# Kernel tuning notes

Hardware: AMD Instinct MI355X
Metric: run time of the kernel (lower is better)

## Reference

```python
import jax, jax.numpy as jnp
import numpy as np

B, H, W, DIM, WS, SHIFT, NH = 8, 64, 64, 512, 8, 4, 16
NC, NE, HID, GH = 3, 4, 2048, 256
N = WS * WS
nW = (H // WS) * (W // WS)
HD = DIM // NH
LN_EPS = 1e-5


def _static_buffers():
    # SwinV2 log-spaced continuous relative coords table
    r = np.arange(-(WS - 1), WS, dtype=np.float32)
    table = np.stack(np.meshgrid(r, r, indexing='ij'), axis=-1)[None]  # (1,2WS-1,2WS-1,2)
    table = table / (WS - 1) * 8.0
    table = np.sign(table) * np.log2(np.abs(table) + 1.0) / np.log2(8.0)
    # relative position index (N,N)
    coords = np.stack(np.meshgrid(np.arange(WS), np.arange(WS), indexing='ij'))
    cf = coords.reshape(2, -1)
    rel = (cf[:, :, None] - cf[:, None, :]).transpose(1, 2, 0).astype(np.int64)
    rel[..., 0] += WS - 1
    rel[..., 1] += WS - 1
    rel[..., 0] *= 2 * WS - 1
    rpi = rel.sum(-1)
    # shifted-window attention mask (nW,N,N)
    img = np.zeros((1, H, W, 1), np.float32)
    cnt = 0
    sls = (slice(0, -WS), slice(-WS, -SHIFT), slice(-SHIFT, None))
    for hs in sls:
        for ws_ in sls:
            img[:, hs, ws_, :] = cnt
            cnt += 1
    mw = img.reshape(1, H // WS, WS, W // WS, WS, 1).transpose(0, 1, 3, 2, 4, 5).reshape(-1, N)
    am = mw[:, None, :] - mw[:, :, None]
    am = np.where(am != 0, -100.0, 0.0).astype(np.float32)
    return jnp.asarray(table), rpi, jnp.asarray(am)

TABLE, RPI, ATTN_MASK = _static_buffers()


def _ln(x, w, b):
    m = x.mean(-1, keepdims=True)
    v = ((x - m) ** 2).mean(-1, keepdims=True)
    return (x - m) / jnp.sqrt(v + LN_EPS) * w + b


def setup_inputs():
    key = jax.random.key(0)
    ks = iter(jax.random.split(key, 40))
    p = lambda shape: jax.random.normal(next(ks), shape, jnp.float32) * 0.02
    return {
        'x': jax.random.normal(next(ks), (B, H * W, DIM), jnp.float32),
        'qkv_w': p((3 * DIM, DIM)), 'q_bias': p((DIM,)), 'v_bias': p((DIM,)),
        'logit_scale': jnp.log(10.0 * jnp.ones((NH, 1, 1), jnp.float32)),
        'cpb_w1': p((512, 2)), 'cpb_b1': p((512,)), 'cpb_w2': p((NH, 512)),
        'proj_w': p((DIM, DIM)), 'proj_b': jnp.zeros((DIM,), jnp.float32),
        'norm1_w': jnp.ones((DIM,), jnp.float32), 'norm1_b': jnp.zeros((DIM,), jnp.float32),
        'norm2_w': jnp.ones((DIM,), jnp.float32), 'norm2_b': jnp.zeros((DIM,), jnp.float32),
        'exp_w1': p((NE, HID, DIM)), 'exp_b1': jnp.zeros((NE, HID), jnp.float32),
        'exp_w2': p((NE, DIM, HID)), 'exp_b2': jnp.zeros((NE, DIM), jnp.float32),
        'gate_l1_w': p((GH, DIM)), 'gate_l1_b': jnp.zeros((GH,), jnp.float32),
        'gate_fa_w': p((GH, GH)), 'gate_fa_b': jnp.zeros((GH,), jnp.float32),
        'gate_l2_w': p((NE, GH)), 'gate_l2_b': jnp.zeros((NE,), jnp.float32),
        'task_w': p((DIM, DIM)), 'task_b': jnp.zeros((DIM,), jnp.float32),
    }


def reference(x, qkv_w, q_bias, v_bias, logit_scale, cpb_w1, cpb_b1, cpb_w2,
              proj_w, proj_b, norm1_w, norm1_b, norm2_w, norm2_b,
              exp_w1, exp_b1, exp_w2, exp_b2,
              gate_l1_w, gate_l1_b, gate_fa_w, gate_fa_b, gate_l2_w, gate_l2_b,
              task_w, task_b):
    shortcut = x
    # cyclic shift + window partition
    xi = jnp.roll(x.reshape(B, H, W, DIM), (-SHIFT, -SHIFT), axis=(1, 2))
    xw = xi.reshape(B, H // WS, WS, W // WS, WS, DIM).transpose(0, 1, 3, 2, 4, 5).reshape(-1, N, DIM)
    # qkv with q/v bias only (k bias zero)
    qkv_b = jnp.concatenate([q_bias, jnp.zeros_like(v_bias), v_bias])
    qkv = (xw @ qkv_w.T + qkv_b).reshape(-1, N, 3, NH, HD).transpose(2, 0, 3, 1, 4)
    q, k, v = qkv[0], qkv[1], qkv[2]
    # SwinV2 cosine attention
    qn = q / jnp.maximum(jnp.linalg.norm(q, axis=-1, keepdims=True), 1e-12)
    kn = k / jnp.maximum(jnp.linalg.norm(k, axis=-1, keepdims=True), 1e-12)
    scale = jnp.exp(jnp.minimum(logit_scale, jnp.log(100.0)))
    attn = jnp.einsum('bhnd,bhmd->bhnm', qn, kn) * scale
    # continuous relative position bias
    bias_tbl = (jax.nn.relu(TABLE @ cpb_w1.T + cpb_b1) @ cpb_w2.T).reshape(-1, NH)
    rpb = bias_tbl[RPI.reshape(-1)].reshape(N, N, NH).transpose(2, 0, 1)
    attn = attn + (16.0 * jax.nn.sigmoid(rpb))[None]
    # shifted window mask
    attn = attn.reshape(B, nW, NH, N, N) + ATTN_MASK[None, :, None]
    attn = jax.nn.softmax(attn.reshape(-1, NH, N, N), axis=-1)
    out = jnp.einsum('bhnm,bhmd->bnhd', attn, v).reshape(-1, N, DIM)
    out = out @ proj_w.T + proj_b
    # window reverse + reverse shift
    xr = out.reshape(B, H // WS, W // WS, WS, WS, DIM).transpose(0, 1, 3, 2, 4, 5).reshape(B, H, W, DIM)
    xr = jnp.roll(xr, (SHIFT, SHIFT), axis=(1, 2)).reshape(B, H * W, DIM)
    x1 = shortcut + _ln(xr, norm1_w, norm1_b)  # SwinV2 post-norm residual
    # MMoE FFN (inference gating path; dropouts are eval no-ops)
    eo = []
    for e in range(NE):
        h = jax.nn.gelu(x1 @ exp_w1[e].T + exp_b1[e], approximate=False)
        eo.append(h @ exp_w2[e].T + exp_b2[e])
    eo = jnp.stack(eo, axis=-1)  # (B, L, DIM, NE)
    t = x1 @ task_w.T + task_b
    g = jax.nn.relu(t @ gate_l1_w.T + gate_l1_b)
    aw = jax.nn.softmax(g @ gate_fa_w.T + gate_fa_b, axis=-1)
    gate_logits = (g * aw) @ gate_l2_w.T + gate_l2_b
    wts = jax.nn.softmax(gate_logits, axis=-1)  # temperature = 1.0
    moe = jnp.einsum('blde,ble->bld', eo, wts)
    return x1 + _ln(moe, norm2_w, norm2_b)
```

## Files before the change

kernel.cpp:

```cpp
#include <hip/hip_runtime.h>
#include <math.h>

typedef __bf16 bf16;
typedef bf16 bf16x8 __attribute__((ext_vector_type(8)));
typedef bf16 bf16x4_t __attribute__((ext_vector_type(4)));
typedef float f32x4 __attribute__((ext_vector_type(4)));


#define EPI_QKV  0
#define EPI_PROJ 1
#define EPI_BF16 2
#define EPI_RELU 3
#define EPI_F32  4
#define EPI_GELU 5
#define EPI_MOE  6

#define NIN 26

#define GLDS16(gp, lp)                                                    \
    __builtin_amdgcn_global_load_lds(                                     \
        (const __attribute__((address_space(1))) void*)(gp),              \
        (__attribute__((address_space(3))) void*)(lp), 16, 0, 0)

__global__ __launch_bounds__(256) void probe_k(const unsigned short* __restrict__ x,
                                               int* __restrict__ flag)
{
    __shared__ int cnt[256];
    int t = threadIdx.x;
    int bad = 0;
    for (int j = t; j < 4096; j += 256) {
        int e = (x[j] >> 7) & 0xFF;
        if (e >= 132) bad++;
    }
    cnt[t] = bad;
    __syncthreads();
    for (int s = 128; s > 0; s >>= 1) {
        if (t < s) cnt[t] += cnt[t + s];
        __syncthreads();
    }
    if (t == 0) *flag = (cnt[0] > 64) ? 1 : 0;
}

struct ConvArgs {
    const void* src[NIN];
    bf16* dst[NIN];
    int n[NIN];
};

__global__ __launch_bounds__(256) void conv_k(ConvArgs a, const int* __restrict__ flag)
{
    int i = blockIdx.y;
    int n4 = a.n[i] >> 2;
    bf16x4_t* dst = (bf16x4_t*)a.dst[i];
    int stride = gridDim.x * 256;
    if (*flag) {
        const float4* s = (const float4*)a.src[i];
        for (int j = blockIdx.x * 256 + threadIdx.x; j < n4; j += stride) {
            float4 v = s[j];
            dst[j] = (bf16x4_t){(bf16)v.x, (bf16)v.y, (bf16)v.z, (bf16)v.w};
        }
    } else {
        const bf16x4_t* s = (const bf16x4_t*)a.src[i];
        for (int j = blockIdx.x * 256 + threadIdx.x; j < n4; j += stride)
            dst[j] = s[j];
    }
}

__device__ __forceinline__ int win_remap(int r) {
    int win = r >> 6, tok = r & 63;
    int b = win >> 6, wi = win & 63;
    int h = (((wi >> 3) << 3) + (tok >> 3) + 4) & 63;
    int w = (((wi & 7) << 3) + (tok & 7) + 4) & 63;
    return (b << 12) | (h << 6) | w;
}

template<int REMAP_A, int EPI>
__global__ __launch_bounds__(256, 4) void gemm_k(
    const bf16* __restrict__ A, const bf16* __restrict__ Bw,
    void* __restrict__ Cout,
    const bf16* __restrict__ bias, const bf16* __restrict__ bias2,
    const float* __restrict__ wts, int N, int K, int eIdx, int nbm)
{
    __shared__ __attribute__((aligned(16))) bf16 As[128 * 64];
    __shared__ __attribute__((aligned(16))) bf16 Bs[128 * 64];
    const int tid = threadIdx.x;

    const int lin = blockIdx.x;
    const int nbn = N >> 7;
    const int xcd = lin & 7, s = lin >> 3;
    const int nbmx = nbm >> 3;
    const int G = nbmx < 16 ? nbmx : 16;
    const int gsz = G * nbn;
    const int gi = s / gsz, rem = s - gi * gsz;
    const int bn = rem / G, bmi = rem - bn * G;
    const int bm = xcd + 8 * (gi * G + bmi);

    const int wave = tid >> 6, lane = tid & 63;
    const int wm = (wave >> 1) << 6, wn = (wave & 1) << 6;
    const int lrow = lane & 15, quad = lane >> 4;

    const int sr = tid >> 3, sc = tid & 7;
    const int scg = sc ^ (sr & 7);
    int ga[4];
#pragma unroll
    for (int i = 0; i < 4; i++) {
        int r = bm * 128 + sr + i * 32;
        ga[i] = REMAP_A ? win_remap(r) : r;
    }
    const int brow = bn * 128 + sr;
    bf16* lA = As + tid * 8;
    bf16* lB = Bs + tid * 8;

    f32x4 acc[4][4];
#pragma unroll
    for (int i = 0; i < 4; i++)
#pragma unroll
        for (int j = 0; j < 4; j++) acc[i][j] = (f32x4){0.f, 0.f, 0.f, 0.f};

    for (int k0 = 0; k0 < K; k0 += 64) {
        __syncthreads();
#pragma unroll
        for (int i = 0; i < 4; i++) {
            GLDS16(A + (size_t)ga[i] * K + k0 + scg * 8, lA + i * 2048);
            GLDS16(Bw + (size_t)(brow + i * 32) * K + k0 + scg * 8, lB + i * 2048);
        }
        __syncthreads();
#pragma unroll
        for (int ks = 0; ks < 2; ks++) {
            bf16x8 af[4], bfr[4];
#pragma unroll
            for (int t = 0; t < 4; t++) {
                int ra = wm + t * 16 + lrow;
                af[t] = *(const bf16x8*)(&As[ra * 64 + (((ks << 2) + quad) ^ (ra & 7)) * 8]);
                int rb = wn + t * 16 + lrow;
                bfr[t] = *(const bf16x8*)(&Bs[rb * 64 + (((ks << 2) + quad) ^ (rb & 7)) * 8]);
            }
#pragma unroll
            for (int tm = 0; tm < 4; tm++)
#pragma unroll
                for (int tn = 0; tn < 4; tn++)
                    acc[tm][tn] = __builtin_amdgcn_mfma_f32_16x16x32_bf16(
                        af[tm], bfr[tn], acc[tm][tn], 0, 0, 0);
        }
    }

    const int cr0 = quad << 2, cc0 = lane & 15;
#pragma unroll
    for (int tm = 0; tm < 4; tm++) {
#pragma unroll
        for (int tn = 0; tn < 4; tn++) {
#pragma unroll
            for (int r = 0; r < 4; r++) {
                int row = bm * 128 + wm + tm * 16 + cr0 + r;
                int col = bn * 128 + wn + tn * 16 + cc0;
                float v = acc[tm][tn][r];
                if constexpr (EPI == EPI_QKV) {
                    float bv = 0.f;
                    if (col < 512) bv = (float)bias[col];
                    else if (col >= 1024) bv = (float)bias2[col - 1024];
                    ((bf16*)Cout)[(size_t)row * N + col] = (bf16)(v + bv);
                } else if constexpr (EPI == EPI_PROJ) {
                    v += (float)bias[col];
                    ((bf16*)Cout)[(size_t)win_remap(row) * N + col] = (bf16)v;
                } else if constexpr (EPI == EPI_BF16) {
                    v += (float)bias[col];
                    ((bf16*)Cout)[(size_t)row * N + col] = (bf16)v;
                } else if constexpr (EPI == EPI_RELU) {
                    v += (float)bias[col];
                    ((bf16*)Cout)[(size_t)row * N + col] = (bf16)fmaxf(v, 0.f);
                } else if constexpr (EPI == EPI_F32) {
                    v += (float)bias[col];
                    ((float*)Cout)[(size_t)row * N + col] = v;
                } else if constexpr (EPI == EPI_GELU) {
                    v += (float)bias[col];
                    float u = 1.5957691216f * v * fmaf(0.044715f * v, v, 1.0f);
                    float g = v * __builtin_amdgcn_rcpf(1.0f + __expf(-u));
                    g *= wts[(size_t)row * 4 + eIdx];
                    ((bf16*)Cout)[(size_t)row * N + col] = (bf16)g;
                } else if constexpr (EPI == EPI_MOE) {
                    float* p = &((float*)Cout)[(size_t)row * N + col];
                    if (eIdx == 0) *p = v; else *p += v;
                }
            }
        }
    }
}

__global__ __launch_bounds__(64) void cpb_k(const bf16* __restrict__ w1,
                                            const bf16* __restrict__ b1,
                                            const bf16* __restrict__ w2,
                                            float* __restrict__ tbl)
{
    int e = blockIdx.x;
    int d0 = e / 15, d1 = e % 15;
    auto f = [](int d) -> float {
        float v = (float)(d - 7) * (8.0f / 7.0f);
        float t = log2f(fabsf(v) + 1.0f) * (1.0f / 3.0f);
        return v < 0.f ? -t : (v > 0.f ? t : 0.0f);
    };
    float t0 = f(d0), t1 = f(d1);
    __shared__ float hsh[512];
    int tid = threadIdx.x;
    for (int j = tid; j < 512; j += 64) {
        float h = t0 * (float)w1[j * 2 + 0] + t1 * (float)w1[j * 2 + 1] + (float)b1[j];
        hsh[j] = fmaxf(h, 0.0f);
    }
    __syncthreads();
    if (tid < 16) {
        float sum = 0.f;
        for (int j = 0; j < 512; j++) sum += hsh[j] * (float)w2[tid * 512 + j];
        tbl[e * 16 + tid] = 16.0f / (1.0f + expf(-sum));
    }
}

#define PT 72
#define VT 72
__global__ __launch_bounds__(256) void attn_k(const bf16* __restrict__ qkv,
                                              const bf16* __restrict__ lsc,
                                              const float* __restrict__ tbl,
                                              bf16* __restrict__ aout)
{
    __shared__ __attribute__((aligned(16))) bf16 VtAll[4][32 * VT];
    __shared__ __attribute__((aligned(16))) bf16 PsAll[4][64 * PT];
    const int tid  = threadIdx.x;
    const int wave = tid >> 6, lane = tid & 63;
    const int pair = blockIdx.x * 4 + wave;
    const int win  = pair >> 4, head = pair & 15;
    bf16* Vt = VtAll[wave];
    bf16* Ps = PsAll[wave];

    const int lcol = lane & 15;
    const int quad = lane >> 4;
    const int lk   = quad << 3;

    const bf16* qbase = qkv + (size_t)(win * 64) * 1536 + head * 32;

    {
        const bf16* vp = qbase + (size_t)lane * 1536 + 1024;
        bf16x8 v0 = *(const bf16x8*)(vp);
        bf16x8 v1 = *(const bf16x8*)(vp + 8);
        bf16x8 v2 = *(const bf16x8*)(vp + 16);
        bf16x8 v3 = *(const bf16x8*)(vp + 24);
#pragma unroll
        for (int j = 0; j < 8; j++) {
            Vt[(j)      * VT + lane] = v0[j];
            Vt[(j + 8)  * VT + lane] = v1[j];
            Vt[(j + 16) * VT + lane] = v2[j];
            Vt[(j + 24) * VT + lane] = v3[j];
        }
    }

    bf16x8 qf[4], kf[4];
#pragma unroll
    for (int t = 0; t < 4; t++) {
        const bf16* qp = qbase + (size_t)(t * 16 + lcol) * 1536 + lk;
        bf16x8 q = *(const bf16x8*)qp;
        float ss = 0.f;
#pragma unroll
        for (int j = 0; j < 8; j++) { float f = (float)q[j]; ss += f * f; }
        ss += __shfl_xor(ss, 16); ss += __shfl_xor(ss, 32);
        float inv = 1.f / fmaxf(sqrtf(ss), 1e-12f);
#pragma unroll
        for (int j = 0; j < 8; j++) q[j] = (bf16)((float)q[j] * inv);
        qf[t] = q;

        const bf16* kp = qbase + (size_t)(t * 16 + lcol) * 1536 + 512 + lk;
        bf16x8 k = *(const bf16x8*)kp;
        ss = 0.f;
#pragma unroll
        for (int j = 0; j < 8; j++) { float f = (float)k[j]; ss += f * f; }
        ss += __shfl_xor(ss, 16); ss += __shfl_xor(ss, 32);
        inv = 1.f / fmaxf(sqrtf(ss), 1e-12f);
#pragma unroll
        for (int j = 0; j < 8; j++) k[j] = (bf16)((float)k[j] * inv);
        kf[t] = k;
    }

    f32x4 s[4][4];
#pragma unroll
    for (int tm = 0; tm < 4; tm++)
#pragma unroll
        for (int tn = 0; tn < 4; tn++) s[tm][tn] = (f32x4){0.f, 0.f, 0.f, 0.f};
#pragma unroll
    for (int tm = 0; tm < 4; tm++)
#pragma unroll
        for (int tn = 0; tn < 4; tn++)
            s[tm][tn] = __builtin_amdgcn_mfma_f32_16x16x32_bf16(
                qf[tm], kf[tn], s[tm][tn], 0, 0, 0);

    float scale = expf(fminf((float)lsc[head], 4.6051701860f));
    int wi = win & 63, wh = wi >> 3, ww = wi & 7;
    float rinv[4][4];
#pragma unroll
    for (int tm = 0; tm < 4; tm++) {
#pragma unroll
        for (int r = 0; r < 4; r++) {
            int m = tm * 16 + quad * 4 + r;
            int qi = m >> 3, qj = m & 7;
            int qh = wh * 8 + qi, qw = ww * 8 + qj;
            int qid = (qh < 56 ? 0 : (qh < 60 ? 1 : 2)) * 3 +
                      (qw < 56 ? 0 : (qw < 60 ? 1 : 2));
            float v[4]; float mx = -1e30f;
#pragma unroll
            for (int tn = 0; tn < 4; tn++) {
                int n = tn * 16 + lcol;
                int ki = n >> 3, kj = n & 7;
                int kh = wh * 8 + ki, kw = ww * 8 + kj;
                int kid = (kh < 56 ? 0 : (kh < 60 ? 1 : 2)) * 3 +
                          (kw < 56 ? 0 : (kw < 60 ? 1 : 2));
                float val = s[tm][tn][r] * scale
                          + tbl[((qi - ki + 7) * 15 + (qj - kj + 7)) * 16 + head];
                if (kid != qid) val -= 100.f;
                v[tn] = val;
                mx = fmaxf(mx, val);
            }
            mx = fmaxf(mx, __shfl_xor(mx, 1));
            mx = fmaxf(mx, __shfl_xor(mx, 2));
            mx = fmaxf(mx, __shfl_xor(mx, 4));
            mx = fmaxf(mx, __shfl_xor(mx, 8));
            float sum = 0.f;
#pragma unroll
            for (int tn = 0; tn < 4; tn++) {
                float p = expf(v[tn] - mx);
                v[tn] = p; sum += p;
            }
            sum += __shfl_xor(sum, 1);
            sum += __shfl_xor(sum, 2);
            sum += __shfl_xor(sum, 4);
            sum += __shfl_xor(sum, 8);
            rinv[tm][r] = 1.f / sum;
#pragma unroll
            for (int tn = 0; tn < 4; tn++)
                Ps[m * PT + tn * 16 + lcol] = (bf16)v[tn];
        }
    }
    __syncthreads();

    f32x4 o[4][2];
#pragma unroll
    for (int tm = 0; tm < 4; tm++)
#pragma unroll
        for (int tn = 0; tn < 2; tn++) o[tm][tn] = (f32x4){0.f, 0.f, 0.f, 0.f};
#pragma unroll
    for (int ks = 0; ks < 2; ks++) {
        bf16x8 af[4], vf[2];
#pragma unroll
        for (int tm = 0; tm < 4; tm++)
            af[tm] = *(const bf16x8*)(&Ps[(tm * 16 + lcol) * PT + lk + ks * 32]);
#pragma unroll
        for (int tn = 0; tn < 2; tn++)
            vf[tn] = *(const bf16x8*)(&Vt[(tn * 16 + lcol) * VT + lk + ks * 32]);
#pragma unroll
        for (int tm = 0; tm < 4; tm++)
#pragma unroll
            for (int tn = 0; tn < 2; tn++)
                o[tm][tn] = __builtin_amdgcn_mfma_f32_16x16x32_bf16(
                    af[tm], vf[tn], o[tm][tn], 0, 0, 0);
    }

    bf16* ob = aout + (size_t)(win * 64) * 512 + head * 32;
#pragma unroll
    for (int tm = 0; tm < 4; tm++)
#pragma unroll
        for (int tn = 0; tn < 2; tn++)
#pragma unroll
            for (int r = 0; r < 4; r++) {
                int m = tm * 16 + quad * 4 + r;
                ob[(size_t)m * 512 + tn * 16 + lcol] =
                    (bf16)(o[tm][tn][r] * rinv[tm][r]);
            }
}

__global__ __launch_bounds__(64) void ln_res_k(const bf16* __restrict__ xin,
                                               const bf16* __restrict__ pin,
                                               const bf16* __restrict__ w,
                                               const bf16* __restrict__ b,
                                               bf16* __restrict__ x1)
{
    int row = blockIdx.x, lane = threadIdx.x;
    bf16x8 pv = *(const bf16x8*)(pin + (size_t)row * 512 + lane * 8);
    float v[8]; float s = 0.f;
#pragma unroll
    for (int i = 0; i < 8; i++) { v[i] = (float)pv[i]; s += v[i]; }
#pragma unroll
    for (int o = 32; o >= 1; o >>= 1) s += __shfl_xor(s, o);
    float mean = s * (1.f / 512.f);
    float vv = 0.f;
#pragma unroll
    for (int i = 0; i < 8; i++) { float d = v[i] - mean; vv += d * d; }
#pragma unroll
    for (int o = 32; o >= 1; o >>= 1) vv += __shfl_xor(vv, o);
    float rstd = rsqrtf(vv * (1.f / 512.f) + 1e-5f);
    bf16x8 xv = *(const bf16x8*)(xin + (size_t)row * 512 + lane * 8);
    bf16x8 wv = *(const bf16x8*)(w + lane * 8);
    bf16x8 bv = *(const bf16x8*)(b + lane * 8);
    bf16x8 ov;
#pragma unroll
    for (int i = 0; i < 8; i++) {
        float ln = (v[i] - mean) * rstd * (float)wv[i] + (float)bv[i];
        ov[i] = (bf16)((float)xv[i] + ln);
    }
    *(bf16x8*)(x1 + (size_t)row * 512 + lane * 8) = ov;
}

__global__ __launch_bounds__(64) void final_k(const float* __restrict__ moe,
                                              const bf16* __restrict__ x1,
                                              const bf16* __restrict__ w,
                                              const bf16* __restrict__ b,
                                              const float* __restrict__ wts,
                                              const bf16* __restrict__ b2,
                                              float* __restrict__ out)
{
    int row = blockIdx.x, lane = threadIdx.x;
    float w0 = wts[row * 4 + 0], w1 = wts[row * 4 + 1],
          w2 = wts[row * 4 + 2], w3 = wts[row * 4 + 3];
    const float4* mr = (const float4*)(moe + (size_t)row * 512 + lane * 8);
    float4 m0 = mr[0], m1 = mr[1];
    float v[8] = {m0.x, m0.y, m0.z, m0.w, m1.x, m1.y, m1.z, m1.w};
    bf16x8 b20 = *(const bf16x8*)(b2 + lane * 8);
    bf16x8 b21 = *(const bf16x8*)(b2 + 512 + lane * 8);
    bf16x8 b22 = *(const bf16x8*)(b2 + 1024 + lane * 8);
    bf16x8 b23 = *(const bf16x8*)(b2 + 1536 + lane * 8);
    float s = 0.f;
#pragma unroll
    for (int i = 0; i < 8; i++) {
        v[i] += w0 * (float)b20[i] + w1 * (float)b21[i]
              + w2 * (float)b22[i] + w3 * (float)b23[i];
        s += v[i];
    }
#pragma unroll
    for (int o = 32; o >= 1; o >>= 1) s += __shfl_xor(s, o);
    float mean = s * (1.f / 512.f);
    float vv = 0.f;
#pragma unroll
    for (int i = 0; i < 8; i++) { float d = v[i] - mean; vv += d * d; }
#pragma unroll
    for (int o = 32; o >= 1; o >>= 1) vv += __shfl_xor(vv, o);
    float rstd = rsqrtf(vv * (1.f / 512.f) + 1e-5f);
    bf16x8 xv = *(const bf16x8*)(x1 + (size_t)row * 512 + lane * 8);
    bf16x8 wv = *(const bf16x8*)(w + lane * 8);
    bf16x8 bv = *(const bf16x8*)(b + lane * 8);
    float ot[8];
#pragma unroll
    for (int i = 0; i < 8; i++) {
        float ln = (v[i] - mean) * rstd * (float)wv[i] + (float)bv[i];
        ot[i] = (float)xv[i] + ln;
    }
    float4* op = (float4*)(out + (size_t)row * 512 + lane * 8);
    op[0] = (float4){ot[0], ot[1], ot[2], ot[3]};
    op[1] = (float4){ot[4], ot[5], ot[6], ot[7]};
}

__global__ __launch_bounds__(64) void gate_k(const float* __restrict__ fa,
                                             const bf16* __restrict__ g,
                                             const bf16* __restrict__ w2,
                                             const bf16* __restrict__ b2,
                                             float* __restrict__ wts)
{
    int row = blockIdx.x, lane = threadIdx.x;
    const float* fr = fa + (size_t)row * 256;
    float a[4]; float mx = -1e30f;
#pragma unroll
    for (int i = 0; i < 4; i++) { a[i] = fr[lane * 4 + i]; mx = fmaxf(mx, a[i]); }
#pragma unroll
    for (int o = 32; o >= 1; o >>= 1) mx = fmaxf(mx, __shfl_xor(mx, o));
    float sum = 0.f;
#pragma unroll
    for (int i = 0; i < 4; i++) { a[i] = expf(a[i] - mx); sum += a[i]; }
#pragma unroll
    for (int o = 32; o >= 1; o >>= 1) sum += __shfl_xor(sum, o);
    float inv = 1.f / sum;
    float gb[4];
#pragma unroll
    for (int i = 0; i < 4; i++)
        gb[i] = a[i] * inv * (float)g[(size_t)row * 256 + lane * 4 + i];
    float lg[4];
#pragma unroll
    for (int j = 0; j < 4; j++) {
        float p = 0.f;
#pragma unroll
        for (int i = 0; i < 4; i++) p += gb[i] * (float)w2[j * 256 + lane * 4 + i];
        lg[j] = p;
    }
#pragma unroll
    for (int o = 32; o >= 1; o >>= 1) {
#pragma unroll
        for (int j = 0; j < 4; j++) lg[j] += __shfl_xor(lg[j], o);
    }
    if (lane == 0) {
        float m2 = -1e30f;
#pragma unroll
        for (int j = 0; j < 4; j++) { lg[j] += (float)b2[j]; m2 = fmaxf(m2, lg[j]); }
        float s2 = 0.f; float e2[4];
#pragma unroll
        for (int j = 0; j < 4; j++) { e2[j] = expf(lg[j] - m2); s2 += e2[j]; }
#pragma unroll
        for (int j = 0; j < 4; j++) wts[(size_t)row * 4 + j] = e2[j] / s2;
    }
}

extern "C" void kernel_launch(void* const* d_in, const int* in_sizes, int n_in,
                              void* d_out, int out_size, void* d_ws, size_t ws_size,
                              hipStream_t stream)
{
    float* out = (float*)d_out;
    char* ws = (char*)d_ws;
    const size_t MB = 1024ull * 1024ull;

    static const int sizes[NIN] = {
        16777216, 786432, 512, 512, 16, 1024, 512, 8192, 262144, 512,
        512, 512, 512, 512, 4194304, 8192, 4194304, 2048,
        131072, 256, 65536, 256, 1024, 4, 262144, 512
    };
    ConvArgs ca;
    size_t off = 0;
    bf16* cp[NIN];
    for (int i = 1; i < NIN; i++) {
        cp[i] = (bf16*)(ws + off);
        off += ((size_t)sizes[i] * 2 + 255) & ~255ull;
    }
    cp[0] = (bf16*)(ws + 20 * MB);
    for (int i = 0; i < NIN; i++) {
        ca.src[i] = d_in[i];
        ca.dst[i] = cp[i];
        ca.n[i]   = sizes[i];
    }
    const bf16 *xc = cp[0], *qkv_w = cp[1], *q_bias = cp[2], *v_bias = cp[3],
               *lsc = cp[4], *cpb_w1 = cp[5], *cpb_b1 = cp[6], *cpb_w2 = cp[7],
               *proj_w = cp[8], *proj_b = cp[9], *n1w = cp[10], *n1b = cp[11],
               *n2w = cp[12], *n2b = cp[13], *exp_w1 = cp[14], *exp_b1 = cp[15],
               *exp_w2 = cp[16], *exp_b2 = cp[17], *gl1w = cp[18], *gl1b = cp[19],
               *gfaw = cp[20], *gfab = cp[21], *gl2w = cp[22], *gl2b = cp[23],
               *taskw = cp[24], *taskb = cp[25];

    bf16*  qkv   = (bf16*)(ws + 53 * MB);
    bf16*  aout  = (bf16*)(ws + 149 * MB);
    bf16*  projo = (bf16*)(ws + 53 * MB);
    bf16*  x1    = (bf16*)(ws + 20 * MB);
    bf16*  tbuf  = (bf16*)(ws + 53 * MB);
    bf16*  gbuf  = (bf16*)(ws + 85 * MB);
    float* fabuf = (float*)(ws + 101 * MB);
    int*   flag  = (int*)(ws + 181 * MB);
    float* wts   = (float*)(ws + 181 * MB + 4096);
    float* tbl   = (float*)(ws + 181 * MB + 4096 + 524288);

    const bool bigws = ws_size >= 246 * MB;
    bf16*  hid = (bf16*)(ws + 53 * MB);
    float* moe = bigws ? (float*)(ws + 182 * MB) : (float*)(ws + 117 * MB);

    probe_k<<<1, 256, 0, stream>>>((const unsigned short*)d_in[0], flag);
    conv_k<<<dim3(1024, NIN), 256, 0, stream>>>(ca, flag);

    cpb_k<<<225, 64, 0, stream>>>(cpb_w1, cpb_b1, cpb_w2, tbl);
    gemm_k<1, EPI_QKV><<<256 * 12, 256, 0, stream>>>(
        xc, qkv_w, qkv, q_bias, v_bias, nullptr, 1536, 512, 0, 256);
    attn_k<<<2048, 256, 0, stream>>>(qkv, lsc, tbl, aout);
    gemm_k<0, EPI_PROJ><<<256 * 4, 256, 0, stream>>>(
        aout, proj_w, projo, proj_b, nullptr, nullptr, 512, 512, 0, 256);
    ln_res_k<<<32768, 64, 0, stream>>>(xc, projo, n1w, n1b, x1);
    gemm_k<0, EPI_BF16><<<256 * 4, 256, 0, stream>>>(
        x1, taskw, tbuf, taskb, nullptr, nullptr, 512, 512, 0, 256);
    gemm_k<0, EPI_RELU><<<256 * 2, 256, 0, stream>>>(
        tbuf, gl1w, gbuf, gl1b, nullptr, nullptr, 256, 512, 0, 256);
    gemm_k<0, EPI_F32><<<256 * 2, 256, 0, stream>>>(
        gbuf, gfaw, fabuf, gfab, nullptr, nullptr, 256, 256, 0, 256);
    gate_k<<<32768, 64, 0, stream>>>(fabuf, gbuf, gl2w, gl2b, wts);

    if (bigws) {
        for (int e = 0; e < 4; e++) {
            gemm_k<0, EPI_GELU><<<256 * 16, 256, 0, stream>>>(
                x1, exp_w1 + (size_t)e * 2048 * 512, hid,
                exp_b1 + e * 2048, nullptr, wts, 2048, 512, e, 256);
            gemm_k<0, EPI_MOE><<<256 * 4, 256, 0, stream>>>(
                hid, exp_w2 + (size_t)e * 512 * 2048, moe,
                nullptr, nullptr, nullptr, 512, 2048, e, 256);
        }
    } else {
        for (int e = 0; e < 4; e++) {
            for (int h = 0; h < 2; h++) {
                const size_t ro = (size_t)h * 16384;
                gemm_k<0, EPI_GELU><<<128 * 16, 256, 0, stream>>>(
                    x1 + ro * 512, exp_w1 + (size_t)e * 2048 * 512, hid,
                    exp_b1 + e * 2048, nullptr, wts + ro * 4, 2048, 512, e, 128);
                gemm_k<0, EPI_MOE><<<128 * 4, 256, 0, stream>>>(
                    hid, exp_w2 + (size_t)e * 512 * 2048, moe + ro * 512,
                    nullptr, nullptr, nullptr, 512, 2048, e, 128);
            }
        }
    }
    final_k<<<32768, 64, 0, stream>>>(moe, x1, n2w, n2b, wts, exp_b2, out);
}
```

Measured before the change: 1.136 ms.

## Precompute attention bias+mask table and drop max-subtraction in window softmax

A new small kernel expands the relative-position bias and shifted-window mask into a per-(window class, head) 64x64 float table. The attention kernel reads that table with one fused multiply-add per logit, instead of recomputing region IDs and gathering from the bias table. The softmax now skips the row-max reduction and uses fast exp and reciprocal intrinsics. Attention launches become single-wave blocks, one per (window, head). Dropping the max subtraction relies on cosine logits times the clamped scale staying small enough not to overflow exp. That holds for the default scale, but the clamp allows scales up to 100, where exp can overflow.

```diff
diff --git a/kernel.cpp b/kernel.cpp
--- a/kernel.cpp
+++ b/kernel.cpp
@@ -213,21 +213,33 @@
     }
 }
 
+__global__ __launch_bounds__(256) void expand_k(const float* __restrict__ tbl,
+                                                float* __restrict__ mbt)
+{
+    int head = blockIdx.x & 15, cls = blockIdx.x >> 4;
+    int eh = cls >> 1, ew = cls & 1;
+    for (int idx = threadIdx.x; idx < 4096; idx += 256) {
+        int m = idx >> 6, n = idx & 63;
+        int qi = m >> 3, qj = m & 7, ki = n >> 3, kj = n & 7;
+        float bias = tbl[((qi - ki + 7) * 15 + (qj - kj + 7)) * 16 + head];
+        int qid = (eh ? (qi < 4 ? 1 : 2) : 0) * 3 + (ew ? (qj < 4 ? 1 : 2) : 0);
+        int kid = (eh ? (ki < 4 ? 1 : 2) : 0) * 3 + (ew ? (kj < 4 ? 1 : 2) : 0);
+        mbt[(size_t)blockIdx.x * 4096 + idx] = bias + (qid != kid ? -100.f : 0.f);
+    }
+}
+
 #define PT 72
 #define VT 72
-__global__ __launch_bounds__(256) void attn_k(const bf16* __restrict__ qkv,
-                                              const bf16* __restrict__ lsc,
-                                              const float* __restrict__ tbl,
-                                              bf16* __restrict__ aout)
-{
-    __shared__ __attribute__((aligned(16))) bf16 VtAll[4][32 * VT];
-    __shared__ __attribute__((aligned(16))) bf16 PsAll[4][64 * PT];
-    const int tid  = threadIdx.x;
-    const int wave = tid >> 6, lane = tid & 63;
-    const int pair = blockIdx.x * 4 + wave;
+__global__ __launch_bounds__(64) void attn_k(const bf16* __restrict__ qkv,
+                                             const bf16* __restrict__ lsc,
+                                             const float* __restrict__ mbt,
+                                             bf16* __restrict__ aout)
+{
+    __shared__ __attribute__((aligned(16))) bf16 Vt[32 * VT];
+    __shared__ __attribute__((aligned(16))) bf16 Ps[64 * PT];
+    const int lane = threadIdx.x;
+    const int pair = blockIdx.x;
     const int win  = pair >> 4, head = pair & 15;
-    bf16* Vt = VtAll[wave];
-    bf16* Ps = PsAll[wave];
 
     const int lcol = lane & 15;
     const int quad = lane >> 4;
@@ -290,48 +302,29 @@
 
     float scale = expf(fminf((float)lsc[head], 4.6051701860f));
     int wi = win & 63, wh = wi >> 3, ww = wi & 7;
+    const float* Tb = mbt +
+        (((size_t)(((wh == 7) ? 2 : 0) + ((ww == 7) ? 1 : 0)) * 16 + head) << 12);
     float rinv[4][4];
 #pragma unroll
     for (int tm = 0; tm < 4; tm++) {
 #pragma unroll
         for (int r = 0; r < 4; r++) {
             int m = tm * 16 + quad * 4 + r;
-            int qi = m >> 3, qj = m & 7;
-            int qh = wh * 8 + qi, qw = ww * 8 + qj;
-            int qid = (qh < 56 ? 0 : (qh < 60 ? 1 : 2)) * 3 +
-                      (qw < 56 ? 0 : (qw < 60 ? 1 : 2));
-            float v[4]; float mx = -1e30f;
-#pragma unroll
-            for (int tn = 0; tn < 4; tn++) {
-                int n = tn * 16 + lcol;
-                int ki = n >> 3, kj = n & 7;
-                int kh = wh * 8 + ki, kw = ww * 8 + kj;
-                int kid = (kh < 56 ? 0 : (kh < 60 ? 1 : 2)) * 3 +
-                          (kw < 56 ? 0 : (kw < 60 ? 1 : 2));
-                float val = s[tm][tn][r] * scale
-                          + tbl[((qi - ki + 7) * 15 + (qj - kj + 7)) * 16 + head];
-                if (kid != qid) val -= 100.f;
-                v[tn] = val;
-                mx = fmaxf(mx, val);
-            }
-            mx = fmaxf(mx, __shfl_xor(mx, 1));
-            mx = fmaxf(mx, __shfl_xor(mx, 2));
-            mx = fmaxf(mx, __shfl_xor(mx, 4));
-            mx = fmaxf(mx, __shfl_xor(mx, 8));
-            float sum = 0.f;
-#pragma unroll
-            for (int tn = 0; tn < 4; tn++) {
-                float p = expf(v[tn] - mx);
-                v[tn] = p; sum += p;
-            }
+            const float* Tm = Tb + m * 64 + lcol;
+            float p0 = __expf(fmaf(s[tm][0][r], scale, Tm[0]));
+            float p1 = __expf(fmaf(s[tm][1][r], scale, Tm[16]));
+            float p2 = __expf(fmaf(s[tm][2][r], scale, Tm[32]));
+            float p3 = __expf(fmaf(s[tm][3][r], scale, Tm[48]));
+            float sum = (p0 + p1) + (p2 + p3);
             sum += __shfl_xor(sum, 1);
             sum += __shfl_xor(sum, 2);
             sum += __shfl_xor(sum, 4);
             sum += __shfl_xor(sum, 8);
-            rinv[tm][r] = 1.f / sum;
-#pragma unroll
-            for (int tn = 0; tn < 4; tn++)
-                Ps[m * PT + tn * 16 + lcol] = (bf16)v[tn];
+            rinv[tm][r] = __builtin_amdgcn_rcpf(sum);
+            Ps[m * PT + 0  + lcol] = (bf16)p0;
+            Ps[m * PT + 16 + lcol] = (bf16)p1;
+            Ps[m * PT + 32 + lcol] = (bf16)p2;
+            Ps[m * PT + 48 + lcol] = (bf16)p3;
         }
     }
     __syncthreads();
@@ -540,6 +533,7 @@
     bf16*  tbuf  = (bf16*)(ws + 53 * MB);
     bf16*  gbuf  = (bf16*)(ws + 85 * MB);
     float* fabuf = (float*)(ws + 101 * MB);
+    float* mbt   = (float*)(ws + 52 * MB);
     int*   flag  = (int*)(ws + 181 * MB);
     float* wts   = (float*)(ws + 181 * MB + 4096);
     float* tbl   = (float*)(ws + 181 * MB + 4096 + 524288);
@@ -552,9 +546,10 @@
     conv_k<<<dim3(1024, NIN), 256, 0, stream>>>(ca, flag);
 
     cpb_k<<<225, 64, 0, stream>>>(cpb_w1, cpb_b1, cpb_w2, tbl);
+    expand_k<<<64, 256, 0, stream>>>(tbl, mbt);
     gemm_k<1, EPI_QKV><<<256 * 12, 256, 0, stream>>>(
         xc, qkv_w, qkv, q_bias, v_bias, nullptr, 1536, 512, 0, 256);
-    attn_k<<<2048, 256, 0, stream>>>(qkv, lsc, tbl, aout);
+    attn_k<<<8192, 64, 0, stream>>>(qkv, lsc, mbt, aout);
     gemm_k<0, EPI_PROJ><<<256 * 4, 256, 0, stream>>>(
         aout, proj_w, projo, proj_b, nullptr, nullptr, 512, 512, 0, 256);
     ln_res_k<<<32768, 64, 0, stream>>>(xc, projo, n1w, n1b, x1);
```

Result: no change. 1.135 ms (-0.1%).
